# Kernel tuning notes

Measured on AMD Instinct MI355X. Metric: run time of the kernel, lower is better.

## Reference

```python
import jax, jax.numpy as jnp
import numpy as np

NUM_HEADS = 16
D_MODEL = 1024
NEG_INF = -1e30


def setup_inputs() -> dict:
    key = jax.random.key(0)
    ks = jax.random.split(key, 7)
    B, S, D = 2, 2048, D_MODEL
    scale = 1.0 / np.sqrt(D)
    return {
        "queries": jax.random.normal(ks[0], (B, S, D), dtype=jnp.float32),
        "keys": jax.random.normal(ks[1], (B, S, D), dtype=jnp.float32),
        "values": jax.random.normal(ks[2], (B, S, D), dtype=jnp.float32),
        "Wq": jax.random.normal(ks[3], (D, D), dtype=jnp.float32) * scale,
        "Wk": jax.random.normal(ks[4], (D, D), dtype=jnp.float32) * scale,
        "Wv": jax.random.normal(ks[5], (D, D), dtype=jnp.float32) * scale,
        "Wo": jax.random.normal(ks[6], (D, D), dtype=jnp.float32) * scale,
    }


def _split_heads(x, h):
    # [B, S, D] -> [B, h, S, D/h]
    B, S, D = x.shape
    return x.reshape(B, S, h, D // h).transpose(0, 2, 1, 3)


def reference(queries, keys, values, Wq, Wk, Wv, Wo):
    h = NUM_HEADS
    q = _split_heads(queries @ Wq, h)  # [B, h, S, dh]
    k = _split_heads(keys @ Wk, h)
    v = _split_heads(values @ Wv, h)
    dh = q.shape[-1]
    scores = jnp.einsum("bhqd,bhkd->bhqk", q, k) / jnp.sqrt(jnp.float32(dh))
    # original quirk: exactly-zero scores are masked to -1e30 before softmax
    scores = jnp.where(scores == 0, NEG_INF, scores)
    attn = jax.nn.softmax(scores, axis=-1)
    out = jnp.einsum("bhqk,bhkd->bhqd", attn, v)  # [B, h, S, dh]
    B, _, S, _ = out.shape
    out = out.transpose(0, 2, 1, 3).reshape(B, S, h * dh)
    return out @ Wo
```

## Files before the change

kernel.cpp:

```cpp
#include <hip/hip_runtime.h>

typedef unsigned short u16;
typedef short bf16x8 __attribute__((ext_vector_type(8)));
typedef float f32x4 __attribute__((ext_vector_type(4)));
typedef float f32x16 __attribute__((ext_vector_type(16)));

namespace {

constexpr int kB = 2, kS = 2048, kD = 1024, kH = 16, kDh = 64;
constexpr float kC2 = 0.125f * 1.44269504088896341f;

__device__ inline u16 f32_bf16(float f) {
    unsigned u = __float_as_uint(f);
    u += 0x7FFFu + ((u >> 16) & 1u);
    return (u16)(u >> 16);
}

__device__ inline float fast_exp2(float x) {
    float r;
    asm("v_exp_f32 %0, %1" : "=v"(r) : "v"(x));
    return r;
}

__device__ inline unsigned cvtpk(float a, float b) {
    unsigned r;
    asm("v_cvt_pk_bf16_f32 %0, %1, %2" : "=v"(r) : "v"(a), "v"(b));
    return r;
}

__device__ inline unsigned pkf16(float a, float b) {
    unsigned r;
    asm("v_cvt_pkrtz_f16_f32 %0, %1, %2" : "=v"(r) : "v"(a), "v"(b));
    return r;
}

__device__ inline void plswap(unsigned& a, unsigned& b) {
    asm("v_permlane32_swap_b32 %0, %1" : "+v"(a), "+v"(b));
}

__device__ inline void gl_lds16(const void* g, void* l) {
    __builtin_amdgcn_global_load_lds(
        (const __attribute__((address_space(1))) void*)g,
        (__attribute__((address_space(3))) void*)l, 16, 0, 0);
}

__device__ inline int swz8(int l) {
    return ((l & 3) ^ ((l >> 2) & 3) ^ ((l >> 4) & 3)) * 8;
}

__global__ __launch_bounds__(256) void prep(
    const float* __restrict__ s0, const float* __restrict__ s1,
    const float* __restrict__ s2,
    u16* __restrict__ d0, u16* __restrict__ d1, u16* __restrict__ d2,
    const float* __restrict__ W0, const float* __restrict__ W1,
    const float* __restrict__ W2, const float* __restrict__ W3,
    u16* __restrict__ T0, u16* __restrict__ T1,
    u16* __restrict__ T2, u16* __restrict__ T3)
{
    const int y = blockIdx.y;
    if (y < 3) {
        const float* src = y == 0 ? s0 : (y == 1 ? s1 : s2);
        u16* dst = y == 0 ? d0 : (y == 1 ? d1 : d2);
        const int i = blockIdx.x * 256 + threadIdx.x;
        const float4* s4 = (const float4*)src;
        float4 a = s4[2 * i], b = s4[2 * i + 1];
        uint4 o;
        o.x = (unsigned)f32_bf16(a.x) | ((unsigned)f32_bf16(a.y) << 16);
        o.y = (unsigned)f32_bf16(a.z) | ((unsigned)f32_bf16(a.w) << 16);
        o.z = (unsigned)f32_bf16(b.x) | ((unsigned)f32_bf16(b.y) << 16);
        o.w = (unsigned)f32_bf16(b.z) | ((unsigned)f32_bf16(b.w) << 16);
        ((uint4*)dst)[i] = o;
        return;
    }
    if (blockIdx.x >= 256) return;
    const int z = y - 3;
    const float* W = z == 0 ? W0 : (z == 1 ? W1 : (z == 2 ? W2 : W3));
    u16* Wt = z == 0 ? T0 : (z == 1 ? T1 : (z == 2 ? T2 : T3));
    const float sc = (z == 0) ? kC2 : 1.0f;

    __shared__ __attribute__((aligned(16))) u16 T[64][65];
    const int t = threadIdx.x;
    const int n0 = (blockIdx.x & 15) * 64, k0 = (blockIdx.x >> 4) * 64;
    const int r = t >> 4, c4 = (t & 15) * 4;
#pragma unroll
    for (int it = 0; it < 4; ++it) {
        const int rr = r + 16 * it;
        float4 v = *(const float4*)(W + (size_t)(k0 + rr) * kD + n0 + c4);
        T[rr][c4 + 0] = f32_bf16(v.x * sc);
        T[rr][c4 + 1] = f32_bf16(v.y * sc);
        T[rr][c4 + 2] = f32_bf16(v.z * sc);
        T[rr][c4 + 3] = f32_bf16(v.w * sc);
    }
    __syncthreads();
#pragma unroll
    for (int it = 0; it < 4; ++it) {
        const int nn = r + 16 * it;
        uint2 pk;
        pk.x = (unsigned)T[c4 + 0][nn] | ((unsigned)T[c4 + 1][nn] << 16);
        pk.y = (unsigned)T[c4 + 2][nn] | ((unsigned)T[c4 + 3][nn] << 16);
        *(uint2*)(Wt + (size_t)(n0 + nn) * kD + k0 + c4) = pk;
    }
}

__global__ __launch_bounds__(256) void vtrans(
    const u16* __restrict__ V, u16* __restrict__ Vt)
{
    __shared__ __attribute__((aligned(16))) u16 T[64][65];
    const int t = threadIdx.x;
    const int s0 = blockIdx.x * 64;
    const int bh = blockIdx.y, b = bh >> 4, h = bh & 15;
    const int rr = t >> 3, c0 = (t & 7) * 8;
    union { u16 u[8]; uint4 v4; } buf;
#pragma unroll
    for (int p = 0; p < 2; ++p) {
        const int s = rr + 32 * p;
        buf.v4 = *(const uint4*)(V + (size_t)(b * kS + s0 + s) * kD + h * kDh + c0);
#pragma unroll
        for (int i = 0; i < 8; ++i) T[c0 + i][s] = buf.u[i];
    }
    __syncthreads();
#pragma unroll
    for (int p = 0; p < 2; ++p) {
        const int d = rr + 32 * p;
#pragma unroll
        for (int i = 0; i < 8; ++i) buf.u[i] = T[d][c0 + i];
        *(uint4*)(Vt + (size_t)(bh * kDh + d) * kS + s0 + c0) = buf.v4;
    }
}

template <bool F32OUT>
__device__ inline void gemm128_body(
    const u16* __restrict__ A, const u16* __restrict__ Wt,
    void* __restrict__ Cout, int M, int N, int K, int bx, int by)
{
    __shared__ __attribute__((aligned(16))) u16 As[128 * 32];
    __shared__ __attribute__((aligned(16))) u16 Bs[128 * 32];
    const int t = threadIdx.x, w = t >> 6, l = t & 63;
    const int quad = l >> 4, c = l & 15;
    const int wm = w >> 1, wn = w & 1;
    const int m0 = by * 128, n0 = bx * 128;
    const int lr = l >> 2, lc = swz8(l);
    const int xc = ((quad ^ (c & 3) ^ ((c >> 2) & 3))) * 8;

    const u16* ga0 = A  + (size_t)(m0 + w * 32 + lr) * K + lc;
    const u16* ga1 = A  + (size_t)(m0 + w * 32 + 16 + lr) * K + lc;
    const u16* gb0 = Wt + (size_t)(n0 + w * 32 + lr) * K + lc;
    const u16* gb1 = Wt + (size_t)(n0 + w * 32 + 16 + lr) * K + lc;
    u16* la0 = &As[(w * 32) * 32];
    u16* la1 = &As[(w * 32 + 16) * 32];
    u16* lb0 = &Bs[(w * 32) * 32];
    u16* lb1 = &Bs[(w * 32 + 16) * 32];

    f32x4 acc[4][4];
#pragma unroll
    for (int mi = 0; mi < 4; ++mi)
#pragma unroll
        for (int nj = 0; nj < 4; ++nj) acc[mi][nj] = 0;

    for (int k0 = 0; k0 < K; k0 += 32) {
        gl_lds16(ga0 + k0, la0);
        gl_lds16(ga1 + k0, la1);
        gl_lds16(gb0 + k0, lb0);
        gl_lds16(gb1 + k0, lb1);
        __syncthreads();
        bf16x8 af[4], bf[4];
#pragma unroll
        for (int mi = 0; mi < 4; ++mi)
            af[mi] = *(const bf16x8*)&As[(wm * 64 + mi * 16 + c) * 32 + xc];
#pragma unroll
        for (int nj = 0; nj < 4; ++nj)
            bf[nj] = *(const bf16x8*)&Bs[(wn * 64 + nj * 16 + c) * 32 + xc];
#pragma unroll
        for (int mi = 0; mi < 4; ++mi)
#pragma unroll
            for (int nj = 0; nj < 4; ++nj)
                acc[mi][nj] = __builtin_amdgcn_mfma_f32_16x16x32_bf16(
                    af[mi], bf[nj], acc[mi][nj], 0, 0, 0);
        __syncthreads();
    }

#pragma unroll
    for (int mi = 0; mi < 4; ++mi)
#pragma unroll
        for (int nj = 0; nj < 4; ++nj)
#pragma unroll
            for (int r = 0; r < 4; ++r) {
                const size_t row = m0 + wm * 64 + mi * 16 + quad * 4 + r;
                const size_t col = n0 + wn * 64 + nj * 16 + c;
                if (F32OUT)
                    ((float*)Cout)[row * N + col] = acc[mi][nj][r];
                else
                    ((u16*)Cout)[row * N + col] = f32_bf16(acc[mi][nj][r]);
            }
}

__global__ __launch_bounds__(256) void gemm_qkv(
    const u16* __restrict__ A0, const u16* __restrict__ A1,
    const u16* __restrict__ A2,
    const u16* __restrict__ W0, const u16* __restrict__ W1,
    const u16* __restrict__ W2,
    u16* __restrict__ C0, u16* __restrict__ C1, u16* __restrict__ C2)
{
    const int z = blockIdx.z;
    const u16* A  = z == 0 ? A0 : (z == 1 ? A1 : A2);
    const u16* Wt = z == 0 ? W0 : (z == 1 ? W1 : W2);
    u16* C = z == 0 ? C0 : (z == 1 ? C1 : C2);
    gemm128_body<false>(A, Wt, C, kB * kS, kD, kD, blockIdx.x, blockIdx.y);
}

__global__ __launch_bounds__(256) void gemm_out(
    const u16* __restrict__ A, const u16* __restrict__ Wt,
    float* __restrict__ C)
{
    __shared__ __attribute__((aligned(16))) u16 As[64 * 32];
    __shared__ __attribute__((aligned(16))) u16 Bs[128 * 32];
    const int N = kD, K = kD;
    const int t = threadIdx.x, w = t >> 6, l = t & 63;
    const int quad = l >> 4, c = l & 15;
    const int wm = w >> 1, wn = w & 1;
    const int m0 = blockIdx.y * 64, n0 = blockIdx.x * 128;
    const int lr = l >> 2, lc = swz8(l);
    const int xc = ((quad ^ (c & 3) ^ ((c >> 2) & 3))) * 8;

    const u16* ga  = A  + (size_t)(m0 + w * 16 + lr) * K + lc;
    const u16* gb0 = Wt + (size_t)(n0 + w * 16 + lr) * K + lc;
    const u16* gb1 = Wt + (size_t)(n0 + 64 + w * 16 + lr) * K + lc;
    u16* la  = &As[(w * 16) * 32];
    u16* lb0 = &Bs[(w * 16) * 32];
    u16* lb1 = &Bs[(64 + w * 16) * 32];

    f32x4 acc[2][4];
#pragma unroll
    for (int mi = 0; mi < 2; ++mi)
#pragma unroll
        for (int nj = 0; nj < 4; ++nj) acc[mi][nj] = 0;

    for (int k0 = 0; k0 < K; k0 += 32) {
        gl_lds16(ga + k0, la);
        gl_lds16(gb0 + k0, lb0);
        gl_lds16(gb1 + k0, lb1);
        __syncthreads();
        bf16x8 af[2], bf[4];
#pragma unroll
        for (int mi = 0; mi < 2; ++mi)
            af[mi] = *(const bf16x8*)&As[(wm * 32 + mi * 16 + c) * 32 + xc];
#pragma unroll
        for (int nj = 0; nj < 4; ++nj)
            bf[nj] = *(const bf16x8*)&Bs[(wn * 64 + nj * 16 + c) * 32 + xc];
#pragma unroll
        for (int mi = 0; mi < 2; ++mi)
#pragma unroll
            for (int nj = 0; nj < 4; ++nj)
                acc[mi][nj] = __builtin_amdgcn_mfma_f32_16x16x32_bf16(
                    af[mi], bf[nj], acc[mi][nj], 0, 0, 0);
        __syncthreads();
    }

#pragma unroll
    for (int mi = 0; mi < 2; ++mi)
#pragma unroll
        for (int nj = 0; nj < 4; ++nj)
#pragma unroll
            for (int r = 0; r < 4; ++r) {
                const size_t row = m0 + wm * 32 + mi * 16 + quad * 4 + r;
                const size_t col = n0 + wn * 64 + nj * 16 + c;
                C[row * N + col] = acc[mi][nj][r];
            }
}

__global__ __launch_bounds__(256) void attn(
    const u16* __restrict__ Q, const u16* __restrict__ K,
    const u16* __restrict__ Vt, u16* __restrict__ PO, float* __restrict__ L)
{
    __shared__ __attribute__((aligned(16))) u16 KsA[64 * 64];
    __shared__ __attribute__((aligned(16))) u16 KsB[64 * 64];
    __shared__ __attribute__((aligned(16))) u16 VtA[64 * 64];
    __shared__ __attribute__((aligned(16))) u16 VtB[64 * 64];

    const int t = threadIdx.x, w = t >> 6, l = t & 63;
    const int half = l >> 5, m = l & 31;
    const int q0 = blockIdx.x * 128;
    const int bh = blockIdx.y, b = bh >> 4, h = bh & 15;
    const int g = blockIdx.z;
    const int sr = l >> 3;
    const int sc = (l & 7) ^ sr;

    const size_t kbase = (size_t)(b * kS) * kD + h * kDh;
    const size_t vbase = (size_t)bh * kDh * kS;
    const int kg0 = g * (kS / 2);

    auto stage = [&](int kt, u16* KsP, u16* VtP) {
#pragma unroll
        for (int i = 0; i < 2; ++i) {
            const int R0 = w * 16 + i * 8;
            gl_lds16(K + kbase + (size_t)(kg0 + kt * 64 + R0 + sr) * kD + sc * 8,
                     &KsP[R0 * 64]);
            gl_lds16(Vt + vbase + (size_t)(R0 + sr) * kS + kg0 + kt * 64 + sc * 8,
                     &VtP[R0 * 64]);
        }
    };

    stage(0, KsA, VtA);

    bf16x8 qf[4];
    {
        const u16* qp = Q + (size_t)(b * kS + q0 + w * 32 + m) * kD
                        + h * kDh + half * 8;
#pragma unroll
        for (int ch = 0; ch < 4; ++ch)
            qf[ch] = *(const bf16x8*)(qp + ch * 16);
    }

    bf16x8 ones;
#pragma unroll
    for (int i = 0; i < 8; ++i) ones[i] = (short)0x3F80;

    f32x16 o0 = 0, o1 = 0;
    f32x16 ol = 0;

    __syncthreads();

    auto compute = [&](const u16* KsP, const u16* VtP) {
        f32x16 s0 = 0, s1 = 0;
        __builtin_amdgcn_s_setprio(1);
#pragma unroll
        for (int ch = 0; ch < 4; ++ch) {
            const int xo = ((2 * ch + half) ^ (m & 7)) * 8;
            const bf16x8 kf0 = *(const bf16x8*)&KsP[(m) * 64 + xo];
            const bf16x8 kf1 = *(const bf16x8*)&KsP[(32 + m) * 64 + xo];
            s0 = __builtin_amdgcn_mfma_f32_32x32x16_bf16(kf0, qf[ch], s0, 0, 0, 0);
            s1 = __builtin_amdgcn_mfma_f32_32x32x16_bf16(kf1, qf[ch], s1, 0, 0, 0);
        }
        __builtin_amdgcn_s_setprio(0);
#pragma unroll
        for (int r = 0; r < 16; ++r) {
            s0[r] = fast_exp2(s0[r]);
            s1[r] = fast_exp2(s1[r]);
        }
        __builtin_amdgcn_s_setprio(1);
#pragma unroll
        for (int ts = 0; ts < 4; ++ts) {
            const int rb = (ts & 1) * 8;
            unsigned c0, c1, c2, c3;
            if (ts < 2) {
                c0 = cvtpk(s0[rb + 0], s0[rb + 1]);
                c1 = cvtpk(s0[rb + 2], s0[rb + 3]);
                c2 = cvtpk(s0[rb + 4], s0[rb + 5]);
                c3 = cvtpk(s0[rb + 6], s0[rb + 7]);
            } else {
                c0 = cvtpk(s1[rb + 0], s1[rb + 1]);
                c1 = cvtpk(s1[rb + 2], s1[rb + 3]);
                c2 = cvtpk(s1[rb + 4], s1[rb + 5]);
                c3 = cvtpk(s1[rb + 6], s1[rb + 7]);
            }
            plswap(c0, c2);
            plswap(c1, c3);
            union { unsigned u[4]; bf16x8 v; } pb;
            pb.u[0] = c0; pb.u[1] = c1; pb.u[2] = c2; pb.u[3] = c3;
            const int xo = ((2 * ts + half) ^ (m & 7)) * 8;
            const bf16x8 vf0 = *(const bf16x8*)&VtP[(m) * 64 + xo];
            const bf16x8 vf1 = *(const bf16x8*)&VtP[(32 + m) * 64 + xo];
            o0 = __builtin_amdgcn_mfma_f32_32x32x16_bf16(vf0, pb.v, o0, 0, 0, 0);
            o1 = __builtin_amdgcn_mfma_f32_32x32x16_bf16(vf1, pb.v, o1, 0, 0, 0);
            ol = __builtin_amdgcn_mfma_f32_32x32x16_bf16(ones, pb.v, ol, 0, 0, 0);
        }
        __builtin_amdgcn_s_setprio(0);
    };

    constexpr int NT = (kS / 2) / 64;
#pragma unroll 1
    for (int kt = 0; kt < NT; kt += 2) {
        if (kt + 1 < NT) stage(kt + 1, KsB, VtB);
        compute(KsA, VtA);
        __syncthreads();
        if (kt + 2 < NT) stage(kt + 2, KsA, VtA);
        compute(KsB, VtB);
        __syncthreads();
    }

    u16* ob = w == 0 ? KsA : (w == 1 ? KsB : (w == 2 ? VtA : VtB));
#pragma unroll
    for (int r = 0; r < 4; ++r) {
        uint2 p0, p1;
        p0.x = pkf16(o0[4 * r + 0], o0[4 * r + 1]);
        p0.y = pkf16(o0[4 * r + 2], o0[4 * r + 3]);
        p1.x = pkf16(o1[4 * r + 0], o1[4 * r + 1]);
        p1.y = pkf16(o1[4 * r + 2], o1[4 * r + 3]);
        *(uint2*)&ob[m * 64 + ((r ^ (m & 7)) << 3) + 4 * half] = p0;
        *(uint2*)&ob[m * 64 + (((4 + r) ^ (m & 7)) << 3) + 4 * half] = p1;
    }
    const size_t srow = (size_t)(g * 32 + bh) * kS + q0 + w * 32;
    if (l < 32) L[srow + l] = ol[0];
#pragma unroll
    for (int i = 0; i < 4; ++i) {
        const int q = l >> 1;
        const int tt = (l & 1) + i * 2;
        uint4 dd = *(const uint4*)&ob[q * 64 + ((tt ^ (q & 7)) << 3)];
        *(uint4*)(PO + (srow + q) * 64 + tt * 8) = dd;
    }
}

__global__ __launch_bounds__(256) void combine(
    const u16* __restrict__ PO, const float* __restrict__ L,
    u16* __restrict__ AO)
{
    typedef _Float16 f16;
    const size_t chunk = (size_t)blockIdx.x * 256 + threadIdx.x;
    const size_t flat = chunk * 8;
    const int bh = (int)(flat >> 17);
    const int s  = (int)((flat >> 6) & 2047);
    const int d  = (int)(flat & 63);
    const float l0 = L[(size_t)bh * kS + s];
    const float l1 = L[(size_t)(32 + bh) * kS + s];
    const float inv = 1.0f / (l0 + l1);
    union { uint4 v; f16 hx[8]; } a, c;
    a.v = *(const uint4*)(PO + flat);
    c.v = *(const uint4*)(PO + (size_t)(32) * kS * 64 + flat);
    unsigned o[4];
#pragma unroll
    for (int j = 0; j < 4; ++j) {
        const float x0 = ((float)a.hx[2 * j]     + (float)c.hx[2 * j])     * inv;
        const float x1 = ((float)a.hx[2 * j + 1] + (float)c.hx[2 * j + 1]) * inv;
        o[j] = (unsigned)f32_bf16(x0) | ((unsigned)f32_bf16(x1) << 16);
    }
    const int b = bh >> 4, h = bh & 15;
    *(uint4*)(AO + ((size_t)(b * kS + s)) * kD + h * kDh + d) = *(uint4*)o;
}

}

extern "C" void kernel_launch(void* const* d_in, const int* in_sizes, int n_in,
                              void* d_out, int out_size, void* d_ws, size_t ws_size,
                              hipStream_t stream)
{
    const float* q_in = (const float*)d_in[0];
    const float* k_in = (const float*)d_in[1];
    const float* v_in = (const float*)d_in[2];
    const float* Wq   = (const float*)d_in[3];
    const float* Wk   = (const float*)d_in[4];
    const float* Wv   = (const float*)d_in[5];
    const float* Wo   = (const float*)d_in[6];

    u16* ws = (u16*)d_ws;
    const size_t M1 = 1u << 20;
    u16* xq  = ws;
    u16* xk  = ws + 4 * M1;
    u16* xv  = ws + 8 * M1;
    u16* Wtq = ws + 12 * M1;
    u16* Wtk = ws + 13 * M1;
    u16* Wtv = ws + 14 * M1;
    u16* Wto = ws + 15 * M1;
    u16* Qp  = ws + 16 * M1;
    u16* Kp  = ws + 20 * M1;
    u16* Vp  = ws + 24 * M1;
    u16* AO  = ws + 28 * M1;
    u16* Vtg = xq;
    u16* PO  = xk;
    float* Lb = (float*)Vp;

    hipLaunchKernelGGL(prep, dim3(2048, 7), dim3(256), 0, stream,
                       q_in, k_in, v_in, xq, xk, xv,
                       Wq, Wk, Wv, Wo, Wtq, Wtk, Wtv, Wto);

    hipLaunchKernelGGL(gemm_qkv, dim3(8, 32, 3), dim3(256), 0, stream,
                       xq, xk, xv, Wtq, Wtk, Wtv, Qp, Kp, Vp);

    hipLaunchKernelGGL(vtrans, dim3(32, 32), dim3(256), 0, stream, Vp, Vtg);

    hipLaunchKernelGGL(attn, dim3(16, 32, 2), dim3(256), 0, stream,
                       Qp, Kp, Vtg, PO, Lb);

    hipLaunchKernelGGL(combine, dim3(2048), dim3(256), 0, stream, PO, Lb, AO);

    hipLaunchKernelGGL(gemm_out, dim3(8, 64), dim3(256), 0, stream,
                       AO, Wto, (float*)d_out);
}
```

Before: 221.8 us.

## Remap attention grid for XCD locality, stage Q in LDS, sum softmax denominators on VALU

Replaces the 3D attention grid with a 1D grid whose block index is decoded so that blocks on the same XCD share a (batch, head), aiming to improve L2 reuse of K/V. Q tiles are now loaded asynchronously into LDS and read per chunk, instead of being held in registers. The row-sum MFMA against a ones vector is dropped in favour of VALU accumulation of the exp values plus a cross-lane shuffle. This frees MFMA issue slots and registers, at the cost of extra LDS traffic and a larger LDS footprint that may reduce occupancy. The row sums now come from the fp32 exp values rather than the bf16-rounded P, which slightly changes the normalisation numerics.

```diff
diff --git a/kernel.cpp b/kernel.cpp
--- a/kernel.cpp
+++ b/kernel.cpp
@@ -276,12 +276,17 @@
     __shared__ __attribute__((aligned(16))) u16 KsB[64 * 64];
     __shared__ __attribute__((aligned(16))) u16 VtA[64 * 64];
     __shared__ __attribute__((aligned(16))) u16 VtB[64 * 64];
+    __shared__ __attribute__((aligned(16))) u16 Qs[4 * 32 * 64];
 
     const int t = threadIdx.x, w = t >> 6, l = t & 63;
     const int half = l >> 5, m = l & 31;
-    const int q0 = blockIdx.x * 128;
-    const int bh = blockIdx.y, b = bh >> 4, h = bh & 15;
-    const int g = blockIdx.z;
+    const int wgid = blockIdx.x;
+    const int xcd = wgid & 7, idx = wgid >> 3;
+    const int bh = xcd + 8 * (idx & 3);
+    const int rest = idx >> 2;
+    const int g = rest & 1;
+    const int q0 = (rest >> 1) * 128;
+    const int b = bh >> 4, h = bh & 15;
     const int sr = l >> 3;
     const int sc = (l & 7) ^ sr;
 
@@ -300,23 +305,17 @@
         }
     };
 
+    {
+        const size_t qbase = (size_t)(b * kS + q0 + w * 32) * kD + h * kDh;
+#pragma unroll
+        for (int i = 0; i < 4; ++i)
+            gl_lds16(Q + qbase + (size_t)(i * 8 + sr) * kD + sc * 8,
+                     &Qs[w * 2048 + i * 512]);
+    }
     stage(0, KsA, VtA);
 
-    bf16x8 qf[4];
-    {
-        const u16* qp = Q + (size_t)(b * kS + q0 + w * 32 + m) * kD
-                        + h * kDh + half * 8;
-#pragma unroll
-        for (int ch = 0; ch < 4; ++ch)
-            qf[ch] = *(const bf16x8*)(qp + ch * 16);
-    }
-
-    bf16x8 ones;
-#pragma unroll
-    for (int i = 0; i < 8; ++i) ones[i] = (short)0x3F80;
-
     f32x16 o0 = 0, o1 = 0;
-    f32x16 ol = 0;
+    f32x4 lsum = 0;
 
     __syncthreads();
 
@@ -326,16 +325,22 @@
 #pragma unroll
         for (int ch = 0; ch < 4; ++ch) {
             const int xo = ((2 * ch + half) ^ (m & 7)) * 8;
+            const bf16x8 qf = *(const bf16x8*)&Qs[w * 2048 + m * 64 + xo];
             const bf16x8 kf0 = *(const bf16x8*)&KsP[(m) * 64 + xo];
             const bf16x8 kf1 = *(const bf16x8*)&KsP[(32 + m) * 64 + xo];
-            s0 = __builtin_amdgcn_mfma_f32_32x32x16_bf16(kf0, qf[ch], s0, 0, 0, 0);
-            s1 = __builtin_amdgcn_mfma_f32_32x32x16_bf16(kf1, qf[ch], s1, 0, 0, 0);
+            s0 = __builtin_amdgcn_mfma_f32_32x32x16_bf16(kf0, qf, s0, 0, 0, 0);
+            s1 = __builtin_amdgcn_mfma_f32_32x32x16_bf16(kf1, qf, s1, 0, 0, 0);
         }
         __builtin_amdgcn_s_setprio(0);
 #pragma unroll
         for (int r = 0; r < 16; ++r) {
             s0[r] = fast_exp2(s0[r]);
             s1[r] = fast_exp2(s1[r]);
+        }
+#pragma unroll
+        for (int r = 0; r < 16; r += 4) {
+            lsum += (f32x4){s0[r], s0[r + 1], s0[r + 2], s0[r + 3]};
+            lsum += (f32x4){s1[r], s1[r + 1], s1[r + 2], s1[r + 3]};
         }
         __builtin_amdgcn_s_setprio(1);
 #pragma unroll
@@ -362,7 +367,6 @@
             const bf16x8 vf1 = *(const bf16x8*)&VtP[(32 + m) * 64 + xo];
             o0 = __builtin_amdgcn_mfma_f32_32x32x16_bf16(vf0, pb.v, o0, 0, 0, 0);
             o1 = __builtin_amdgcn_mfma_f32_32x32x16_bf16(vf1, pb.v, o1, 0, 0, 0);
-            ol = __builtin_amdgcn_mfma_f32_32x32x16_bf16(ones, pb.v, ol, 0, 0, 0);
         }
         __builtin_amdgcn_s_setprio(0);
     };
@@ -377,6 +381,9 @@
         compute(KsB, VtB);
         __syncthreads();
     }
+
+    float lt = lsum[0] + lsum[1] + lsum[2] + lsum[3];
+    lt += __shfl_xor(lt, 32, 64);
 
     u16* ob = w == 0 ? KsA : (w == 1 ? KsB : (w == 2 ? VtA : VtB));
 #pragma unroll
@@ -390,7 +397,7 @@
         *(uint2*)&ob[m * 64 + (((4 + r) ^ (m & 7)) << 3) + 4 * half] = p1;
     }
     const size_t srow = (size_t)(g * 32 + bh) * kS + q0 + w * 32;
-    if (l < 32) L[srow + l] = ol[0];
+    if (l < 32) L[srow + l] = lt;
 #pragma unroll
     for (int i = 0; i < 4; ++i) {
         const int q = l >> 1;
@@ -467,7 +474,7 @@
 
     hipLaunchKernelGGL(vtrans, dim3(32, 32), dim3(256), 0, stream, Vp, Vtg);
 
-    hipLaunchKernelGGL(attn, dim3(16, 32, 2), dim3(256), 0, stream,
+    hipLaunchKernelGGL(attn, dim3(1024), dim3(256), 0, stream,
                        Qp, Kp, Vtg, PO, Lb);
 
     hipLaunchKernelGGL(combine, dim3(2048), dim3(256), 0, stream, PO, Lb, AO);
```

Result: no change. 223.4 us (+0.7%).
